# Performance work log

Hardware: AMD Instinct MI355X
Metric: run time of the kernel (lower is better)

## Reference

```python
import jax, jax.numpy as jnp
import numpy as np
import math

B, T, D_MODEL, H = 2, 2048, 1024, 16
HD = D_MODEL // H  # head_dim = 64


def setup_inputs() -> dict:
    key = jax.random.key(0)
    ks = jax.random.split(key, 9)
    inp = {
        "x_q": jax.random.normal(ks[0], (B, T, D_MODEL), dtype=jnp.float32),
        "x_k": jax.random.normal(ks[1], (B, T, D_MODEL), dtype=jnp.float32),
        "x_v": jax.random.normal(ks[2], (B, T, D_MODEL), dtype=jnp.float32),
        "mask": jax.random.randint(ks[3], (B, T), 0, 2, dtype=jnp.int32),
        "causal": 1,
        "relative_position_bias": jax.random.normal(ks[4], (1, H, T, T), dtype=jnp.float32),
        "Wq": jax.random.normal(ks[5], (D_MODEL, D_MODEL), dtype=jnp.float32) * 0.02,
        "Wk": jax.random.normal(ks[6], (D_MODEL, D_MODEL), dtype=jnp.float32) * 0.02,
        "Wv": jax.random.normal(ks[7], (D_MODEL, D_MODEL), dtype=jnp.float32) * 0.02,
        "Wo": jax.random.normal(ks[8], (D_MODEL, D_MODEL), dtype=jnp.float32) * 0.02,
    }
    return inp


def _split_heads(x):
    b, t, _ = x.shape
    return x.reshape(b, t, H, HD).transpose(0, 2, 1, 3)  # (B, H, T, HD)


def reference(x_q, x_k, x_v, mask, causal, relative_position_bias, Wq, Wk, Wv, Wo):
    # torch.nn.Linear: y = x @ W.T
    q = _split_heads(x_q @ Wq.T)
    k = _split_heads(x_k @ Wk.T)
    v = _split_heads(x_v @ Wv.T)

    # padding mask (B, T_k) -> (B, 1, 1, T_k), combined with causal tril
    attn_mask = mask[:, None, None, :]
    if causal:
        tril = jnp.tril(jnp.ones((T, T), dtype=jnp.int32))[None, None]
        attn_mask = attn_mask & tril

    scores = jnp.einsum('bhqd,bhkd->bhqk', q, k) / math.sqrt(HD)
    scores = scores + relative_position_bias
    scores = jnp.where(attn_mask == 0, jnp.float32(-1e9), scores)
    attn = jax.nn.softmax(scores, axis=-1)  # (B, H, Tq, Tk)

    out_h = jnp.einsum('bhqk,bhkd->bhqd', attn, v)
    out = out_h.transpose(0, 2, 1, 3).reshape(B, T, D_MODEL)
    out = out @ Wo.T
    return out, attn
```

## Files before the change

kernel.cpp:

```cpp
#include <hip/hip_runtime.h>
#include <hip/hip_bf16.h>
#include <hip/hip_fp16.h>

#define B_ 2
#define T_ 2048
#define DM 1024
#define H_ 16
#define HD_ 64

typedef __attribute__((ext_vector_type(8))) short bf16x8v;
typedef __attribute__((ext_vector_type(4))) short short4v;
typedef __attribute__((ext_vector_type(4))) float f32x4;

__device__ __forceinline__ short f2bf(float f){
  unsigned u = __builtin_bit_cast(unsigned, f);
  u += 0x7fffu + ((u >> 16) & 1u);
  return (short)(u >> 16);
}
__device__ __forceinline__ float bf2f(short s){
  unsigned u = ((unsigned)(unsigned short)s) << 16;
  return __builtin_bit_cast(float, u);
}
__device__ __forceinline__ short f2h(float f){
  return __builtin_bit_cast(short, __float2half(f));
}
__device__ __forceinline__ float h2f(short s){
  return __half2float(__builtin_bit_cast(__half, s));
}

#define GLOAD_LDS16(g, l) \
  __builtin_amdgcn_global_load_lds((const __attribute__((address_space(1))) unsigned int*)(g), \
                                   (__attribute__((address_space(3))) unsigned int*)(l), 16, 0, 0)

#define MFMA16(a, b, c) __builtin_amdgcn_mfma_f32_16x16x32_bf16((a), (b), (c), 0, 0, 0)

__global__ __launch_bounds__(256) void conv_kernel(
    const float* __restrict__ s0, const float* __restrict__ s1, const float* __restrict__ s2,
    const float* __restrict__ s3, const float* __restrict__ s4, const float* __restrict__ s5,
    const float* __restrict__ s6,
    short* __restrict__ d0, short* __restrict__ d1, short* __restrict__ d2,
    short* __restrict__ d3, short* __restrict__ d4, short* __restrict__ d5,
    short* __restrict__ d6)
{
  int y = blockIdx.y;
  const float* s; short* d; int n;
  switch (y) {
    case 0: s = s0; d = d0; n = B_*T_*DM; break;
    case 1: s = s1; d = d1; n = B_*T_*DM; break;
    case 2: s = s2; d = d2; n = B_*T_*DM; break;
    case 3: s = s3; d = d3; n = DM*DM;   break;
    case 4: s = s4; d = d4; n = DM*DM;   break;
    case 5: s = s5; d = d5; n = DM*DM;   break;
    default: s = s6; d = d6; n = DM*DM;  break;
  }
  int i = (blockIdx.x * 256 + threadIdx.x) * 4;
  if (i >= n) return;
  float4 f = *(const float4*)(s + i);
  short4v o;
  o.x = f2bf(f.x); o.y = f2bf(f.y); o.z = f2bf(f.z); o.w = f2bf(f.w);
  *(short4v*)(d + i) = o;
}

__global__ __launch_bounds__(256) void proj_gemm(
    const short* __restrict__ xq, const short* __restrict__ xk, const short* __restrict__ xv,
    const short* __restrict__ wq, const short* __restrict__ wk, const short* __restrict__ wv,
    short* __restrict__ qo, short* __restrict__ ko, short* __restrict__ vto)
{
  __shared__ short As[128 * 32];
  __shared__ short Bs[128 * 32];
  const int z = blockIdx.z;
  const short* A  = (z == 0) ? xq : (z == 1) ? xk : xv;
  const short* Bw = (z == 0) ? wq : (z == 1) ? wk : wv;
  const int m0 = blockIdx.x * 128;
  const int n0 = blockIdx.y * 128;
  const int tid = threadIdx.x;
  const int w = tid >> 6, l = tid & 63;
  const int wr = w >> 1, wc = w & 1;
  const int fr = l & 15, kq8 = (l >> 4) * 8;
  const int srow = tid >> 2, scol = (tid & 3) * 8;

  f32x4 acc[4][4] = {};

  for (int k0 = 0; k0 < DM; k0 += 32) {
    __syncthreads();
    GLOAD_LDS16(A  + (size_t)(m0 + srow) * DM + k0 + scol,      (char*)As + tid * 16);
    GLOAD_LDS16(A  + (size_t)(m0 + 64 + srow) * DM + k0 + scol, (char*)As + 4096 + tid * 16);
    GLOAD_LDS16(Bw + (size_t)(n0 + srow) * DM + k0 + scol,      (char*)Bs + tid * 16);
    GLOAD_LDS16(Bw + (size_t)(n0 + 64 + srow) * DM + k0 + scol, (char*)Bs + 4096 + tid * 16);
    __syncthreads();
    bf16x8v a[4], b[4];
#pragma unroll
    for (int i = 0; i < 4; i++) a[i] = *(const bf16x8v*)&As[(wr * 64 + i * 16 + fr) * 32 + kq8];
#pragma unroll
    for (int j = 0; j < 4; j++) b[j] = *(const bf16x8v*)&Bs[(wc * 64 + j * 16 + fr) * 32 + kq8];
#pragma unroll
    for (int i = 0; i < 4; i++)
#pragma unroll
      for (int j = 0; j < 4; j++)
        acc[i][j] = MFMA16(a[i], b[j], acc[i][j]);
  }

  const float scale = (z == 0) ? 0.125f : 1.0f;
  short* dst01 = (z == 0) ? qo : ko;
#pragma unroll
  for (int i = 0; i < 4; i++) {
#pragma unroll
    for (int j = 0; j < 4; j++) {
#pragma unroll
      for (int r = 0; r < 4; r++) {
        int row = m0 + wr * 64 + i * 16 + (l >> 4) * 4 + r;
        int col = n0 + wc * 64 + j * 16 + fr;
        int bb = row >> 11, tt = row & (T_ - 1);
        int hh = col >> 6,  hd = col & (HD_ - 1);
        short v = f2bf(acc[i][j][r] * scale);
        if (z == 2)
          vto[(((size_t)bb * H_ + hh) * HD_ + hd) * T_ + tt] = v;
        else
          dst01[(((size_t)bb * H_ + hh) * T_ + tt) * HD_ + hd] = v;
      }
    }
  }
}

__global__ __launch_bounds__(256) void vsum_kernel(const short* __restrict__ vt,
                                                   float* __restrict__ vs)
{
  __shared__ float red[256];
  int bh = blockIdx.x;
  int tid = threadIdx.x;
  int hd = tid & 63, part = tid >> 6;
  const short* src = vt + ((size_t)bh * HD_ + hd) * T_ + part * 512;
  float s = 0.f;
  for (int i = 0; i < 512; i += 4) {
    short4v v = *(const short4v*)(src + i);
    s += bf2f(v.x) + bf2f(v.y) + bf2f(v.z) + bf2f(v.w);
  }
  red[tid] = s;
  __syncthreads();
  if (part == 0)
    vs[(size_t)bh * HD_ + hd] = red[hd] + red[64 + hd] + red[128 + hd] + red[192 + hd];
}

__global__ __launch_bounds__(512, 6) void attn_kernel(
    const short* __restrict__ qw, const short* __restrict__ kw, const short* __restrict__ vt,
    const float* __restrict__ bias, const int* __restrict__ mask,
    const int* __restrict__ causal_p, const float* __restrict__ vsum,
    float* __restrict__ attn_out, short* __restrict__ outh)
{
  __shared__ short s_lds[8 * 2048];
  __shared__ unsigned char mk_lds[T_];
  __shared__ float m_lds[8], l_lds[8];
  __shared__ float pv_lds[2][8][64];

  const int b  = blockIdx.x;
  const int q0 = blockIdx.y * 8;
  const int h  = blockIdx.z;
  const int tid = threadIdx.x;
  const int w = tid >> 6, l = tid & 63;
  const int causal = *causal_p;
  const int L = causal ? (q0 + 8) : T_;
  const int Lpad = (L + 31) & ~31;
  const int fr = l & 15, kq8 = (l >> 4) * 8;

  for (int i = tid; i < T_; i += 512)
    mk_lds[i] = (unsigned char)(mask[b * T_ + i] != 0);
  __syncthreads();

  {
    bf16x8v qf[2];
#pragma unroll
    for (int ks = 0; ks < 2; ks++)
      qf[ks] = *(const bf16x8v*)&qw[(((size_t)b * H_ + h) * T_ + q0 + (fr & 7)) * HD_ + ks * 32 + kq8];

    for (int nt = 0; nt < 16; ++nt) {
      int k0 = (nt * 8 + w) * 16;
      if (k0 >= L) break;
      f32x4 acc = {0.f, 0.f, 0.f, 0.f};
      const short* kb = &kw[(((size_t)b * H_ + h) * T_ + k0 + fr) * HD_ + kq8];
      acc = MFMA16(qf[0], *(const bf16x8v*)kb, acc);
      acc = MFMA16(qf[1], *(const bf16x8v*)(kb + 32), acc);
      if ((l >> 4) < 2) {
        int colg = k0 + fr;
        unsigned char mk = mk_lds[colg];
        const float* bp = bias + ((size_t)h * T_ + q0 + (l >> 4) * 4) * T_ + colg;
#pragma unroll
        for (int r = 0; r < 4; r++) {
          int qrel = (l >> 4) * 4 + r;
          float bi = bp[r * T_];
          bool cok = (!causal) || (colg <= q0 + qrel);
          float s = (mk && cok) ? (acc[r] + bi) : -1e9f;
          *(short*)((char*)s_lds + ((qrel * 4096 + colg * 2) ^ ((qrel & 7) << 4))) = f2h(s);
        }
      }
    }
  }
  __syncthreads();

  {
    int row = w;
    float mx = -3e38f;
    for (int c = l * 8; c < L; c += 512) {
      int byte = (row * 4096 + c * 2) ^ ((row & 7) << 4);
      bf16x8v v = *(const bf16x8v*)((char*)s_lds + byte);
#pragma unroll
      for (int i = 0; i < 8; i++) mx = fmaxf(mx, h2f(v[i]));
    }
#pragma unroll
    for (int off = 1; off < 64; off <<= 1) mx = fmaxf(mx, __shfl_xor(mx, off));
    float sm = 0.f;
    for (int c = l * 8; c < L; c += 512) {
      int byte = (row * 4096 + c * 2) ^ ((row & 7) << 4);
      bf16x8v v = *(const bf16x8v*)((char*)s_lds + byte);
#pragma unroll
      for (int i = 0; i < 8; i++) sm += __expf(h2f(v[i]) - mx);
    }
#pragma unroll
    for (int off = 1; off < 64; off <<= 1) sm += __shfl_xor(sm, off);
    if (l == 0) { m_lds[row] = mx; l_lds[row] = sm; }
  }
  __syncthreads();

  {
    int row = w;
    int qg = q0 + row;
    float mx = m_lds[row];
    bool fullmask = (mx <= -0.5e9f);
    float inv = fullmask ? 0.f : (1.0f / l_lds[row]);
    float fillv = fullmask ? (1.0f / (float)T_) : 0.f;
    float* arow = attn_out + (((size_t)b * H_ + h) * T_ + qg) * T_;
    for (int c = l * 8; c < Lpad; c += 512) {
      int byte = (row * 4096 + c * 2) ^ ((row & 7) << 4);
      if (c < L) {
        bf16x8v v = *(const bf16x8v*)((char*)s_lds + byte);
        float p[8];
#pragma unroll
        for (int i = 0; i < 8; i++)
          p[i] = fullmask ? 0.f : __expf(h2f(v[i]) - mx) * inv;
        f32x4 o0 = {fullmask ? fillv : p[0], fullmask ? fillv : p[1],
                    fullmask ? fillv : p[2], fullmask ? fillv : p[3]};
        f32x4 o1 = {fullmask ? fillv : p[4], fullmask ? fillv : p[5],
                    fullmask ? fillv : p[6], fullmask ? fillv : p[7]};
        __builtin_nontemporal_store(o0, (f32x4*)(arow + c));
        __builtin_nontemporal_store(o1, (f32x4*)(arow + c + 4));
        bf16x8v pb;
#pragma unroll
        for (int i = 0; i < 8; i++) pb[i] = f2bf(p[i]);
        *(bf16x8v*)((char*)s_lds + byte) = pb;
      } else {
        bf16x8v zz = {0, 0, 0, 0, 0, 0, 0, 0};
        *(bf16x8v*)((char*)s_lds + byte) = zz;
      }
    }
    f32x4 f4 = {fillv, fillv, fillv, fillv};
    for (int c = L + l * 8; c < T_; c += 512) {
      __builtin_nontemporal_store(f4, (f32x4*)(arow + c));
      __builtin_nontemporal_store(f4, (f32x4*)(arow + c + 4));
    }
  }
  __syncthreads();

  {
    int half = w >> 2;
    int hd0  = (w & 3) * 16;
    int split = (Lpad / 2) & ~31;
    int kbeg = half ? split : 0;
    int kend = half ? Lpad  : split;
    f32x4 acc = {0.f, 0.f, 0.f, 0.f};
    const short* vb = vt + (((size_t)b * H_ + h) * HD_ + hd0 + fr) * T_;
    int arow = fr & 7;
    for (int k0 = kbeg; k0 < kend; k0 += 32) {
      int byte = (arow * 4096 + (k0 + kq8) * 2) ^ ((arow & 7) << 4);
      bf16x8v pa = *(const bf16x8v*)((char*)s_lds + byte);
      bf16x8v vv = *(const bf16x8v*)(vb + k0 + kq8);
      acc = MFMA16(pa, vv, acc);
    }
    if ((l >> 4) < 2) {
#pragma unroll
      for (int r = 0; r < 4; r++)
        pv_lds[half][(l >> 4) * 4 + r][hd0 + fr] = acc[r];
    }
  }
  __syncthreads();
  {
    int row = tid >> 6, hd = tid & 63;
    float val = pv_lds[0][row][hd] + pv_lds[1][row][hd];
    if (m_lds[row] <= -0.5e9f)
      val = vsum[((size_t)b * H_ + h) * HD_ + hd] * (1.0f / (float)T_);
    outh[(((size_t)b * H_ + h) * T_ + q0 + row) * HD_ + hd] = f2bf(val);
  }
}

__global__ __launch_bounds__(256) void out_gemm(
    const short* __restrict__ Ah, const short* __restrict__ Bw, float* __restrict__ Co)
{
  __shared__ short As[128 * 32];
  __shared__ short Bs[128 * 32];
  const int m0 = blockIdx.x * 128;
  const int n0 = blockIdx.y * 128;
  const int tid = threadIdx.x;
  const int w = tid >> 6, l = tid & 63;
  const int wr = w >> 1, wc = w & 1;
  const int fr = l & 15, kq8 = (l >> 4) * 8;
  const int srow = tid >> 2, scol = (tid & 3) * 8;

  f32x4 acc[4][4] = {};

  for (int k0 = 0; k0 < DM; k0 += 32) {
    __syncthreads();
    int kk = k0 + scol;
    int hh = kk >> 6, hd = kk & 63;
    {
      int m1 = m0 + srow;
      const short* src1 = Ah + (((size_t)(m1 >> 11) * H_ + hh) * T_ + (m1 & (T_ - 1))) * HD_ + hd;
      GLOAD_LDS16(src1, (char*)As + tid * 16);
      int m2 = m0 + 64 + srow;
      const short* src2 = Ah + (((size_t)(m2 >> 11) * H_ + hh) * T_ + (m2 & (T_ - 1))) * HD_ + hd;
      GLOAD_LDS16(src2, (char*)As + 4096 + tid * 16);
    }
    GLOAD_LDS16(Bw + (size_t)(n0 + srow) * DM + kk,      (char*)Bs + tid * 16);
    GLOAD_LDS16(Bw + (size_t)(n0 + 64 + srow) * DM + kk, (char*)Bs + 4096 + tid * 16);
    __syncthreads();
    bf16x8v a[4], b[4];
#pragma unroll
    for (int i = 0; i < 4; i++) a[i] = *(const bf16x8v*)&As[(wr * 64 + i * 16 + fr) * 32 + kq8];
#pragma unroll
    for (int j = 0; j < 4; j++) b[j] = *(const bf16x8v*)&Bs[(wc * 64 + j * 16 + fr) * 32 + kq8];
#pragma unroll
    for (int i = 0; i < 4; i++)
#pragma unroll
      for (int j = 0; j < 4; j++)
        acc[i][j] = MFMA16(a[i], b[j], acc[i][j]);
  }

#pragma unroll
  for (int i = 0; i < 4; i++)
#pragma unroll
    for (int j = 0; j < 4; j++)
#pragma unroll
      for (int r = 0; r < 4; r++) {
        int row = m0 + wr * 64 + i * 16 + (l >> 4) * 4 + r;
        int col = n0 + wc * 64 + j * 16 + fr;
        Co[(size_t)row * DM + col] = acc[i][j][r];
      }
}

extern "C" void kernel_launch(void* const* d_in, const int* in_sizes, int n_in,
                              void* d_out, int out_size, void* d_ws, size_t ws_size,
                              hipStream_t stream)
{
  const float* x_q  = (const float*)d_in[0];
  const float* x_k  = (const float*)d_in[1];
  const float* x_v  = (const float*)d_in[2];
  const int*   mask = (const int*)d_in[3];
  const int*   causal = (const int*)d_in[4];
  const float* bias = (const float*)d_in[5];
  const float* Wq   = (const float*)d_in[6];
  const float* Wk   = (const float*)d_in[7];
  const float* Wv   = (const float*)d_in[8];
  const float* Wo   = (const float*)d_in[9];

  char* ws = (char*)d_ws;
  const size_t XB = (size_t)B_ * T_ * DM * 2;
  const size_t WB = (size_t)DM * DM * 2;
  short* xq_b = (short*)(ws + 0 * XB);
  short* xk_b = (short*)(ws + 1 * XB);
  short* xv_b = (short*)(ws + 2 * XB);
  short* wq_b = (short*)(ws + 3 * XB + 0 * WB);
  short* wk_b = (short*)(ws + 3 * XB + 1 * WB);
  short* wv_b = (short*)(ws + 3 * XB + 2 * WB);
  short* wo_b = (short*)(ws + 3 * XB + 3 * WB);
  short* q_ws  = (short*)(ws + 3 * XB + 4 * WB);
  short* k_ws  = (short*)(ws + 4 * XB + 4 * WB);
  short* vt_ws = (short*)(ws + 5 * XB + 4 * WB);
  short* oh_ws = (short*)(ws + 6 * XB + 4 * WB);
  float* vs_ws = (float*)(ws + 7 * XB + 4 * WB);

  float* out0 = (float*)d_out;
  float* attn = out0 + (size_t)B_ * T_ * DM;

  conv_kernel<<<dim3(4096, 7, 1), 256, 0, stream>>>(
      x_q, x_k, x_v, Wq, Wk, Wv, Wo,
      xq_b, xk_b, xv_b, wq_b, wk_b, wv_b, wo_b);

  proj_gemm<<<dim3(32, 8, 3), 256, 0, stream>>>(
      xq_b, xk_b, xv_b, wq_b, wk_b, wv_b, q_ws, k_ws, vt_ws);

  vsum_kernel<<<dim3(32, 1, 1), 256, 0, stream>>>(vt_ws, vs_ws);

  attn_kernel<<<dim3(B_, T_ / 8, H_), 512, 0, stream>>>(
      q_ws, k_ws, vt_ws, bias, mask, causal, vs_ws, attn, oh_ws);

  out_gemm<<<dim3(32, 8, 1), 256, 0, stream>>>(oh_ws, wo_b, out0);
}
```

Before: 463.3 us.

## Restructure attention into per-wave 16-row tiles with two-pass online softmax

Replaces the block-of-8-queries attention kernel, which staged full fp16 score rows in LDS, with a per-wave 16-query tile design. Each wave first runs an online max/sum pass over the keys, then recomputes scores, normalizes, writes attn probabilities, and accumulates P·V via MFMA on 64-key chunks. Causal tiles are interleaved across waves (qt = w*32 + blockIdx.x) to balance work. The aim is full MFMA tile use (16 rows instead of 8 of 16) and no large LDS score buffer. The cost is that QK^T and the bias loads are done twice.

```diff
diff --git a/kernel.cpp b/kernel.cpp
--- a/kernel.cpp
+++ b/kernel.cpp
@@ -20,12 +20,6 @@
 __device__ __forceinline__ float bf2f(short s){
   unsigned u = ((unsigned)(unsigned short)s) << 16;
   return __builtin_bit_cast(float, u);
-}
-__device__ __forceinline__ short f2h(float f){
-  return __builtin_bit_cast(short, __float2half(f));
-}
-__device__ __forceinline__ float h2f(short s){
-  return __half2float(__builtin_bit_cast(__half, s));
 }
 
 #define GLOAD_LDS16(g, l) \
@@ -141,152 +135,165 @@
     vs[(size_t)bh * HD_ + hd] = red[hd] + red[64 + hd] + red[128 + hd] + red[192 + hd];
 }
 
-__global__ __launch_bounds__(512, 6) void attn_kernel(
+__global__ __launch_bounds__(256, 4) void attn_kernel(
     const short* __restrict__ qw, const short* __restrict__ kw, const short* __restrict__ vt,
     const float* __restrict__ bias, const int* __restrict__ mask,
     const int* __restrict__ causal_p, const float* __restrict__ vsum,
     float* __restrict__ attn_out, short* __restrict__ outh)
 {
-  __shared__ short s_lds[8 * 2048];
-  __shared__ unsigned char mk_lds[T_];
-  __shared__ float m_lds[8], l_lds[8];
-  __shared__ float pv_lds[2][8][64];
-
-  const int b  = blockIdx.x;
-  const int q0 = blockIdx.y * 8;
-  const int h  = blockIdx.z;
+  __shared__ float s_t[4][16][68];
+  __shared__ short p_l[4][16][72];
+  __shared__ float fm_l[4][16];
+
   const int tid = threadIdx.x;
   const int w = tid >> 6, l = tid & 63;
+  const int fr = l & 15, q4 = l >> 4, kq8 = q4 * 8;
+  const int b = blockIdx.y, h = blockIdx.z;
+  const int qt = w * 32 + blockIdx.x;
+  const int q0w = qt * 16;
   const int causal = *causal_p;
-  const int L = causal ? (q0 + 8) : T_;
-  const int Lpad = (L + 31) & ~31;
-  const int fr = l & 15, kq8 = (l >> 4) * 8;
-
-  for (int i = tid; i < T_; i += 512)
-    mk_lds[i] = (unsigned char)(mask[b * T_ + i] != 0);
-  __syncthreads();
-
+  const int L = causal ? (q0w + 16) : T_;
+  const int KEND = (L + 63) & ~63;
+  const size_t bh = (size_t)b * H_ + h;
+  const short* Kb = kw + bh * T_ * HD_;
+  const short* Vb = vt + bh * HD_ * T_;
+  const int* mrow = mask + b * T_;
+  const float* biasb = bias + ((size_t)h * T_ + q0w) * T_;
+  float* arowb = attn_out + (bh * T_ + q0w) * T_;
+  const float invT = 1.0f / (float)T_;
+
+  bf16x8v qa0, qa1;
   {
-    bf16x8v qf[2];
-#pragma unroll
-    for (int ks = 0; ks < 2; ks++)
-      qf[ks] = *(const bf16x8v*)&qw[(((size_t)b * H_ + h) * T_ + q0 + (fr & 7)) * HD_ + ks * 32 + kq8];
-
-    for (int nt = 0; nt < 16; ++nt) {
-      int k0 = (nt * 8 + w) * 16;
-      if (k0 >= L) break;
-      f32x4 acc = {0.f, 0.f, 0.f, 0.f};
-      const short* kb = &kw[(((size_t)b * H_ + h) * T_ + k0 + fr) * HD_ + kq8];
-      acc = MFMA16(qf[0], *(const bf16x8v*)kb, acc);
-      acc = MFMA16(qf[1], *(const bf16x8v*)(kb + 32), acc);
-      if ((l >> 4) < 2) {
-        int colg = k0 + fr;
-        unsigned char mk = mk_lds[colg];
-        const float* bp = bias + ((size_t)h * T_ + q0 + (l >> 4) * 4) * T_ + colg;
-#pragma unroll
-        for (int r = 0; r < 4; r++) {
-          int qrel = (l >> 4) * 4 + r;
-          float bi = bp[r * T_];
-          bool cok = (!causal) || (colg <= q0 + qrel);
-          float s = (mk && cok) ? (acc[r] + bi) : -1e9f;
-          *(short*)((char*)s_lds + ((qrel * 4096 + colg * 2) ^ ((qrel & 7) << 4))) = f2h(s);
-        }
+    const short* qp = qw + (bh * T_ + q0w + fr) * HD_;
+    qa0 = *(const bf16x8v*)(qp + kq8);
+    qa1 = *(const bf16x8v*)(qp + 32 + kq8);
+  }
+
+  float m4[4], l4[4];
+#pragma unroll
+  for (int r = 0; r < 4; r++) { m4[r] = -3e38f; l4[r] = 0.f; }
+
+  for (int k0 = 0; k0 < KEND; k0 += 64) {
+    f32x4 s[4] = {};
+#pragma unroll
+    for (int t = 0; t < 4; t++) {
+      const short* kp = Kb + (size_t)(k0 + t * 16 + fr) * HD_ + kq8;
+      bf16x8v kf0 = *(const bf16x8v*)kp;
+      bf16x8v kf1 = *(const bf16x8v*)(kp + 32);
+      s[t] = MFMA16(qa0, kf0, s[t]);
+      s[t] = MFMA16(qa1, kf1, s[t]);
+      int kcol = k0 + t * 16 + fr;
+      int mk = mrow[kcol];
+      const float* bp = biasb + (size_t)(q4 * 4) * T_ + kcol;
+#pragma unroll
+      for (int r = 0; r < 4; r++) {
+        float bi = bp[(size_t)r * T_];
+        bool ok = (mk != 0) && (!causal || kcol <= q0w + q4 * 4 + r);
+        s[t][r] = ok ? (s[t][r] + bi) : -1e9f;
       }
     }
-  }
-  __syncthreads();
-
-  {
-    int row = w;
-    float mx = -3e38f;
-    for (int c = l * 8; c < L; c += 512) {
-      int byte = (row * 4096 + c * 2) ^ ((row & 7) << 4);
-      bf16x8v v = *(const bf16x8v*)((char*)s_lds + byte);
-#pragma unroll
-      for (int i = 0; i < 8; i++) mx = fmaxf(mx, h2f(v[i]));
-    }
-#pragma unroll
-    for (int off = 1; off < 64; off <<= 1) mx = fmaxf(mx, __shfl_xor(mx, off));
-    float sm = 0.f;
-    for (int c = l * 8; c < L; c += 512) {
-      int byte = (row * 4096 + c * 2) ^ ((row & 7) << 4);
-      bf16x8v v = *(const bf16x8v*)((char*)s_lds + byte);
-#pragma unroll
-      for (int i = 0; i < 8; i++) sm += __expf(h2f(v[i]) - mx);
-    }
-#pragma unroll
-    for (int off = 1; off < 64; off <<= 1) sm += __shfl_xor(sm, off);
-    if (l == 0) { m_lds[row] = mx; l_lds[row] = sm; }
-  }
-  __syncthreads();
-
-  {
-    int row = w;
-    int qg = q0 + row;
-    float mx = m_lds[row];
-    bool fullmask = (mx <= -0.5e9f);
-    float inv = fullmask ? 0.f : (1.0f / l_lds[row]);
-    float fillv = fullmask ? (1.0f / (float)T_) : 0.f;
-    float* arow = attn_out + (((size_t)b * H_ + h) * T_ + qg) * T_;
-    for (int c = l * 8; c < Lpad; c += 512) {
-      int byte = (row * 4096 + c * 2) ^ ((row & 7) << 4);
-      if (c < L) {
-        bf16x8v v = *(const bf16x8v*)((char*)s_lds + byte);
-        float p[8];
-#pragma unroll
-        for (int i = 0; i < 8; i++)
-          p[i] = fullmask ? 0.f : __expf(h2f(v[i]) - mx) * inv;
-        f32x4 o0 = {fullmask ? fillv : p[0], fullmask ? fillv : p[1],
-                    fullmask ? fillv : p[2], fullmask ? fillv : p[3]};
-        f32x4 o1 = {fullmask ? fillv : p[4], fullmask ? fillv : p[5],
-                    fullmask ? fillv : p[6], fullmask ? fillv : p[7]};
-        __builtin_nontemporal_store(o0, (f32x4*)(arow + c));
-        __builtin_nontemporal_store(o1, (f32x4*)(arow + c + 4));
-        bf16x8v pb;
-#pragma unroll
-        for (int i = 0; i < 8; i++) pb[i] = f2bf(p[i]);
-        *(bf16x8v*)((char*)s_lds + byte) = pb;
-      } else {
-        bf16x8v zz = {0, 0, 0, 0, 0, 0, 0, 0};
-        *(bf16x8v*)((char*)s_lds + byte) = zz;
+#pragma unroll
+    for (int r = 0; r < 4; r++) {
+      float tmax = fmaxf(fmaxf(s[0][r], s[1][r]), fmaxf(s[2][r], s[3][r]));
+      float nm = fmaxf(m4[r], tmax);
+      float sc = __expf(m4[r] - nm);
+      float sum = __expf(s[0][r] - nm) + __expf(s[1][r] - nm) +
+                  __expf(s[2][r] - nm) + __expf(s[3][r] - nm);
+      l4[r] = l4[r] * sc + sum;
+      m4[r] = nm;
+    }
+  }
+#pragma unroll
+  for (int r = 0; r < 4; r++) {
+#pragma unroll
+    for (int off = 1; off < 16; off <<= 1) {
+      float om = __shfl_xor(m4[r], off);
+      float ol = __shfl_xor(l4[r], off);
+      float nm = fmaxf(m4[r], om);
+      l4[r] = l4[r] * __expf(m4[r] - nm) + ol * __expf(om - nm);
+      m4[r] = nm;
+    }
+  }
+  float inv4[4];
+#pragma unroll
+  for (int r = 0; r < 4; r++) inv4[r] = 1.0f / l4[r];
+  if (fr == 0) {
+#pragma unroll
+    for (int r = 0; r < 4; r++) fm_l[w][q4 * 4 + r] = m4[r];
+  }
+
+  f32x4 oacc[4] = {};
+  for (int k0 = 0; k0 < KEND; k0 += 64) {
+    f32x4 s[4] = {};
+#pragma unroll
+    for (int t = 0; t < 4; t++) {
+      const short* kp = Kb + (size_t)(k0 + t * 16 + fr) * HD_ + kq8;
+      bf16x8v kf0 = *(const bf16x8v*)kp;
+      bf16x8v kf1 = *(const bf16x8v*)(kp + 32);
+      s[t] = MFMA16(qa0, kf0, s[t]);
+      s[t] = MFMA16(qa1, kf1, s[t]);
+      int kcol = k0 + t * 16 + fr;
+      int mk = mrow[kcol];
+      const float* bp = biasb + (size_t)(q4 * 4) * T_ + kcol;
+#pragma unroll
+      for (int r = 0; r < 4; r++) {
+        float bi = bp[(size_t)r * T_];
+        bool ok = (mk != 0) && (!causal || kcol <= q0w + q4 * 4 + r);
+        s[t][r] = ok ? (s[t][r] + bi) : -1e9f;
       }
     }
-    f32x4 f4 = {fillv, fillv, fillv, fillv};
-    for (int c = L + l * 8; c < T_; c += 512) {
-      __builtin_nontemporal_store(f4, (f32x4*)(arow + c));
-      __builtin_nontemporal_store(f4, (f32x4*)(arow + c + 4));
-    }
-  }
-  __syncthreads();
-
-  {
-    int half = w >> 2;
-    int hd0  = (w & 3) * 16;
-    int split = (Lpad / 2) & ~31;
-    int kbeg = half ? split : 0;
-    int kend = half ? Lpad  : split;
-    f32x4 acc = {0.f, 0.f, 0.f, 0.f};
-    const short* vb = vt + (((size_t)b * H_ + h) * HD_ + hd0 + fr) * T_;
-    int arow = fr & 7;
-    for (int k0 = kbeg; k0 < kend; k0 += 32) {
-      int byte = (arow * 4096 + (k0 + kq8) * 2) ^ ((arow & 7) << 4);
-      bf16x8v pa = *(const bf16x8v*)((char*)s_lds + byte);
-      bf16x8v vv = *(const bf16x8v*)(vb + k0 + kq8);
-      acc = MFMA16(pa, vv, acc);
-    }
-    if ((l >> 4) < 2) {
+#pragma unroll
+    for (int t = 0; t < 4; t++)
 #pragma unroll
       for (int r = 0; r < 4; r++)
-        pv_lds[half][(l >> 4) * 4 + r][hd0 + fr] = acc[r];
-    }
-  }
-  __syncthreads();
-  {
-    int row = tid >> 6, hd = tid & 63;
-    float val = pv_lds[0][row][hd] + pv_lds[1][row][hd];
-    if (m_lds[row] <= -0.5e9f)
-      val = vsum[((size_t)b * H_ + h) * HD_ + hd] * (1.0f / (float)T_);
-    outh[(((size_t)b * H_ + h) * T_ + q0 + row) * HD_ + hd] = f2bf(val);
+        s_t[w][q4 * 4 + r][t * 16 + fr] = __expf(s[t][r] - m4[r]) * inv4[r];
+#pragma unroll
+    for (int j = 0; j < 4; j++) {
+      int row = 4 * j + q4;
+      f32x4 pv = *(const f32x4*)&s_t[w][row][fr * 4];
+      bool fmj = fm_l[w][row] <= -0.5e9f;
+      f32x4 ov;
+      ov[0] = fmj ? invT : pv[0];
+      ov[1] = fmj ? invT : pv[1];
+      ov[2] = fmj ? invT : pv[2];
+      ov[3] = fmj ? invT : pv[3];
+      __builtin_nontemporal_store(ov, (f32x4*)(arowb + (size_t)row * T_ + k0 + fr * 4));
+      short4v pb;
+      pb.x = f2bf(pv[0]); pb.y = f2bf(pv[1]); pb.z = f2bf(pv[2]); pb.w = f2bf(pv[3]);
+      *(short4v*)&p_l[w][row][fr * 4] = pb;
+    }
+#pragma unroll
+    for (int ks = 0; ks < 2; ks++) {
+      bf16x8v pa = *(const bf16x8v*)&p_l[w][fr][ks * 32 + kq8];
+#pragma unroll
+      for (int n0 = 0; n0 < 4; n0++) {
+        bf16x8v vv = *(const bf16x8v*)&Vb[(size_t)(n0 * 16 + fr) * T_ + k0 + ks * 32 + kq8];
+        oacc[n0] = MFMA16(pa, vv, oacc[n0]);
+      }
+    }
+  }
+
+#pragma unroll
+  for (int n0 = 0; n0 < 4; n0++) {
+#pragma unroll
+    for (int r = 0; r < 4; r++) {
+      int row = q4 * 4 + r, col = n0 * 16 + fr;
+      float val = oacc[n0][r];
+      if (m4[r] <= -0.5e9f) val = vsum[bh * HD_ + col] * invT;
+      outh[(bh * T_ + q0w + row) * HD_ + col] = f2bf(val);
+    }
+  }
+
+  if (KEND < T_) {
+#pragma unroll
+    for (int j = 0; j < 4; j++) {
+      int row = 4 * j + q4;
+      float fill = (fm_l[w][row] <= -0.5e9f) ? invT : 0.f;
+      f32x4 fv = {fill, fill, fill, fill};
+      float* rp = arowb + (size_t)row * T_;
+      for (int c = KEND + fr * 4; c < T_; c += 64)
+        __builtin_nontemporal_store(fv, (f32x4*)(rp + c));
+    }
   }
 }
 
@@ -387,7 +394,7 @@
 
   vsum_kernel<<<dim3(32, 1, 1), 256, 0, stream>>>(vt_ws, vs_ws);
 
-  attn_kernel<<<dim3(B_, T_ / 8, H_), 512, 0, stream>>>(
+  attn_kernel<<<dim3(T_ / 16 / 4, B_, H_), 256, 0, stream>>>(
       q_ws, k_ws, vt_ws, bias, mask, causal, vs_ws, attn, oh_ws);
 
   out_gemm<<<dim3(32, 8, 1), 256, 0, stream>>>(oh_ws, wo_b, out0);
```

Measured after the change: 624.9 us. 1.35x slower.
